# Kernel optimization log

Hardware: AMD Instinct MI355X
Metric: run time of the kernel (lower is better)

## Reference

```python
import jax, jax.numpy as jnp
import numpy as np

S, D, H, DK, DV = 4096, 1024, 16, 64, 64


def setup_inputs() -> dict:
    key = jax.random.key(0)
    ks = jax.random.split(key, 6)
    x = jax.random.normal(ks[0], (S, D), dtype=jnp.float32)
    # per-head projection weights, stacked over heads; scaled for numerical sanity
    Wq = jax.random.normal(ks[1], (H, D, DK), dtype=jnp.float32) / np.sqrt(D)
    Wk = jax.random.normal(ks[2], (H, D, DK), dtype=jnp.float32) / np.sqrt(D)
    Wv = jax.random.normal(ks[3], (H, D, DV), dtype=jnp.float32) / np.sqrt(D)
    Wc = jax.random.normal(ks[4], (H * DV, D), dtype=jnp.float32) / np.sqrt(H * DV)
    bc = jnp.zeros((D,), dtype=jnp.float32)
    return {"x": x, "Wq": Wq, "Wk": Wk, "Wv": Wv, "Wc": Wc, "bc": bc}


def reference(x, Wq, Wk, Wv, Wc, bc):
    # Per-head projections (original loops over heads with separate Linears;
    # stacking over h is the same math, vectorized).
    q = jnp.einsum("sd,hdk->hsk", x, Wq)   # [H,S,DK]
    k = jnp.einsum("sd,hdk->hsk", x, Wk)   # [H,S,DK]
    v = jnp.einsum("sd,hdv->hsv", x, Wv)   # [H,S,DV]
    scores = jnp.einsum("hsk,htk->hst", q, k) / jnp.sqrt(jnp.asarray(DK, x.dtype))
    probs = jax.nn.softmax(scores, axis=-1)  # softmax over last dim, per row
    o = jnp.einsum("hst,htv->hsv", probs, v)  # [H,S,DV]
    cat = jnp.transpose(o, (1, 0, 2)).reshape(S, H * DV)  # concat heads on last dim
    return cat @ Wc + bc  # output projection with bias
```

## Files before the change

kernel.cpp:

```cpp
#include <hip/hip_runtime.h>
#include <hip/hip_bf16.h>

#define S_ 4096
#define D_ 1024
#define H_ 16
#define DK_ 64
#define DV_ 64

typedef short bf16x8 __attribute__((ext_vector_type(8)));
typedef float floatx4 __attribute__((ext_vector_type(4)));
using bf16 = __hip_bfloat16;

#define MFMA16(a, b, c) __builtin_amdgcn_mfma_f32_16x16x32_bf16(a, b, c, 0, 0, 0)

#if __has_builtin(__builtin_amdgcn_exp2f)
#define EXP2(x) __builtin_amdgcn_exp2f(x)
#else
#define EXP2(x) exp2f(x)
#endif

__device__ __forceinline__ void stage16(const void* g, void* l) {
    __builtin_amdgcn_global_load_lds(
        (const __attribute__((address_space(1))) void*)g,
        (__attribute__((address_space(3))) void*)l, 16, 0, 0);
}

__device__ __forceinline__ bf16x8 ldsfrag(const bf16* base, int row, int chunk) {
    return *(const bf16x8*)(base + row * 64 + (((chunk ^ (row & 7))) << 3));
}
__device__ __forceinline__ bf16x8 ldsfrag32(const bf16* base, int row, int chunk) {
    return *(const bf16x8*)(base + row * 32 + (((chunk ^ (row & 3))) << 3));
}

__device__ __forceinline__ unsigned short bfbits(float f) {
    union { bf16 h; unsigned short u; } c; c.h = __float2bfloat16(f); return c.u;
}

__global__ __launch_bounds__(256)
void prep(const float* __restrict__ x, const float* __restrict__ Wq,
          const float* __restrict__ Wk, const float* __restrict__ Wv,
          const float* __restrict__ Wc,
          bf16* __restrict__ xb, bf16* __restrict__ Wt, bf16* __restrict__ Wct)
{
    __shared__ float ls[64][65];
    const int bx = blockIdx.x, t = threadIdx.x;

    if (bx < 2048) {
        int i = bx * 2048 + t * 8;
        float4 a = *(const float4*)(x + i);
        float4 b = *(const float4*)(x + i + 4);
        ushort4 lo, hi;
        lo.x = bfbits(a.x); lo.y = bfbits(a.y); lo.z = bfbits(a.z); lo.w = bfbits(a.w);
        hi.x = bfbits(b.x); hi.y = bfbits(b.y); hi.z = bfbits(b.z); hi.w = bfbits(b.w);
        *(ushort4*)(xb + i) = lo;
        *(ushort4*)(xb + i + 4) = hi;
        return;
    }
    if (bx < 2816) {
        const int idx = bx - 2048;
        const int z = idx >> 4, which = z >> 4, h = z & 15;
        const float* s = (which == 0 ? Wq : which == 1 ? Wk : Wv) + (size_t)h * D_ * 64;
        bf16* d = Wt + ((size_t)which * 1024 + h * 64) * D_;
        const float scale = (which == 0) ? 0.125f * 1.44269504088896340736f : 1.0f;
        const int r0 = (idx & 15) * 64;
        {
            int r = t >> 2, cseg = (t & 3) * 16;
            const float* sp = s + (size_t)(r0 + r) * 64 + cseg;
            #pragma unroll
            for (int i = 0; i < 16; i += 4) {
                float4 v = *(const float4*)(sp + i);
                ls[r][cseg + i + 0] = v.x; ls[r][cseg + i + 1] = v.y;
                ls[r][cseg + i + 2] = v.z; ls[r][cseg + i + 3] = v.w;
            }
        }
        __syncthreads();
        {
            int c = t >> 2, rseg = (t & 3) * 16;
            bf16* dp = d + (size_t)c * D_ + r0 + rseg;
            #pragma unroll
            for (int i = 0; i < 16; i++) dp[i] = __float2bfloat16(ls[rseg + i][c] * scale);
        }
        return;
    }
    {
        const int idx = bx - 2816;
        const int r0 = (idx & 15) * 64, c0 = (idx >> 4) * 64;
        {
            int r = t >> 2, cseg = (t & 3) * 16;
            const float* sp = Wc + (size_t)(r0 + r) * D_ + c0 + cseg;
            #pragma unroll
            for (int i = 0; i < 16; i += 4) {
                float4 v = *(const float4*)(sp + i);
                ls[r][cseg + i + 0] = v.x; ls[r][cseg + i + 1] = v.y;
                ls[r][cseg + i + 2] = v.z; ls[r][cseg + i + 3] = v.w;
            }
        }
        __syncthreads();
        {
            int c = t >> 2, rseg = (t & 3) * 16;
            bf16* dp = Wct + (size_t)(c0 + c) * D_ + r0 + rseg;
            #pragma unroll
            for (int i = 0; i < 16; i++) dp[i] = __float2bfloat16(ls[rseg + i][c]);
        }
    }
}

__global__ __launch_bounds__(256)
void qkv_gemm(const bf16* __restrict__ xb, const bf16* __restrict__ Wt,
              bf16* __restrict__ Qb, bf16* __restrict__ Kb, bf16* __restrict__ Vtb)
{
    const int m0 = blockIdx.x * 128;
    const int n0 = blockIdx.y * 128;
    __shared__ __align__(16) bf16 xa[2][128 * 32];
    __shared__ __align__(16) bf16 wb2[2][128 * 32];

    const int t = threadIdx.x, lane = t & 63, w = t >> 6;
    const int l15 = lane & 15, quad = lane >> 4;

    auto stage_a = [&](int buf, int kk) {
        #pragma unroll
        for (int j = 0; j < 2; j++) {
            int row = j * 64 + (t >> 2);
            int ch  = (t & 3) ^ (row & 3);
            stage16((const char*)xb + ((size_t)(m0 + row) * D_ + kk) * 2 + ch * 16,
                    (char*)&xa[buf][0] + (j * 4 + w) * 1024);
        }
    };
    auto stage_b = [&](int buf, int kk) {
        #pragma unroll
        for (int j = 0; j < 2; j++) {
            int row = j * 64 + (t >> 2);
            int ch  = (t & 3) ^ (row & 3);
            stage16((const char*)Wt + ((size_t)(n0 + row) * D_ + kk) * 2 + ch * 16,
                    (char*)&wb2[buf][0] + (j * 4 + w) * 1024);
        }
    };

    const floatx4 fz = {0.f, 0.f, 0.f, 0.f};
    floatx4 acc[2][8];
    #pragma unroll
    for (int mt = 0; mt < 2; mt++)
        #pragma unroll
        for (int nt = 0; nt < 8; nt++) acc[mt][nt] = fz;

    stage_a(0, 0); stage_b(0, 0);
    for (int kt = 0; kt < 32; kt++) {
        int cur = kt & 1;
        __syncthreads();
        if (kt < 31) { stage_a(cur ^ 1, (kt + 1) * 32); stage_b(cur ^ 1, (kt + 1) * 32); }
        bf16x8 a0 = ldsfrag32(&xa[cur][0], w * 32 + l15,      quad);
        bf16x8 a1 = ldsfrag32(&xa[cur][0], w * 32 + 16 + l15, quad);
        #pragma unroll
        for (int nt = 0; nt < 8; nt++) {
            bf16x8 b = ldsfrag32(&wb2[cur][0], nt * 16 + l15, quad);
            acc[0][nt] = MFMA16(a0, b, acc[0][nt]);
            acc[1][nt] = MFMA16(a1, b, acc[1][nt]);
        }
    }

    const int which = n0 >> 10;
    #pragma unroll
    for (int nt = 0; nt < 8; nt++) {
        int n = n0 + nt * 16 + l15;
        int hh = (n >> 6) & 15, col = n & 63;
        #pragma unroll
        for (int mt = 0; mt < 2; mt++)
            #pragma unroll
            for (int r = 0; r < 4; r++) {
                int s = m0 + w * 32 + mt * 16 + quad * 4 + r;
                bf16 val = __float2bfloat16(acc[mt][nt][r]);
                if (which == 0)      Qb[((size_t)hh * S_ + s) * 64 + col] = val;
                else if (which == 1) Kb[((size_t)hh * S_ + s) * 64 + col] = val;
                else                 Vtb[((size_t)hh * 64 + col) * S_ + s] = val;
            }
    }
}

template<int NKT, bool FULL>
__global__ __launch_bounds__(256, 4)
void attn(const bf16* __restrict__ Qb, const bf16* __restrict__ Kb,
          const bf16* __restrict__ Vtb, bf16* __restrict__ Cat,
          float* __restrict__ Opart, float* __restrict__ lpart)
{
    const int m0 = blockIdx.x * 128;
    const int h  = blockIdx.y;
    const int half = blockIdx.z;
    const int keybase = half * (NKT * 32);

    __shared__ __align__(16) bf16 ka[2][32 * 64];
    __shared__ __align__(16) bf16 vt[2][64 * 32];
    __shared__ __align__(16) bf16 pl[128 * 32];

    const int t = threadIdx.x, lane = t & 63, w = t >> 6;
    const int l15 = lane & 15, quad = lane >> 4;

    auto stage_kv = [&](int buf, int key0) {
        {
            int row = t >> 3;
            int ch  = (t & 7) ^ (row & 7);
            stage16((const char*)(Kb + ((size_t)h * S_ + key0) * 64)
                        + (size_t)row * 128 + ch * 16,
                    (char*)&ka[buf][0] + w * 1024);
        }
        {
            int row = t >> 2;
            int ch  = (t & 3) ^ (row & 3);
            stage16((const char*)(Vtb + (size_t)h * 64 * S_ + key0)
                        + (size_t)row * (S_ * 2) + ch * 16,
                    (char*)&vt[buf][0] + w * 1024);
        }
    };

    bf16x8 qf[2][2];
    #pragma unroll
    for (int nq = 0; nq < 2; nq++)
        #pragma unroll
        for (int ks = 0; ks < 2; ks++)
            qf[nq][ks] = *(const bf16x8*)(Qb +
                ((size_t)h * S_ + m0 + w * 32 + nq * 16 + l15) * 64 + ks * 32 + quad * 8);

    const floatx4 fz = {0.f, 0.f, 0.f, 0.f};
    floatx4 acc[2][4];
    float rs[2] = {0.f, 0.f};
    #pragma unroll
    for (int mt = 0; mt < 2; mt++)
        #pragma unroll
        for (int nt = 0; nt < 4; nt++) acc[mt][nt] = fz;

    const int fq = (l15 >> 2) & 3;
    const int prd0 = (w * 32 + l15) * 64 + ((quad ^ fq) << 4);
    const int prd1 = (w * 32 + 16 + l15) * 64 + ((quad ^ fq) << 4);

    stage_kv(0, keybase);
    __syncthreads();

    for (int kt = 0; kt < NKT; kt++) {
        const int cur = kt & 1;
        if (kt + 1 < NKT) stage_kv(cur ^ 1, keybase + (kt + 1) * 32);

        floatx4 sc[2][2];
        #pragma unroll
        for (int mk = 0; mk < 2; mk++)
            #pragma unroll
            for (int nq = 0; nq < 2; nq++) sc[mk][nq] = fz;
        #pragma unroll
        for (int ks = 0; ks < 2; ks++) {
            bf16x8 af0 = ldsfrag(&ka[cur][0],      l15, ks * 4 + quad);
            bf16x8 af1 = ldsfrag(&ka[cur][0], 16 + l15, ks * 4 + quad);
            #pragma unroll
            for (int nq = 0; nq < 2; nq++) {
                sc[0][nq] = MFMA16(af0, qf[nq][ks], sc[0][nq]);
                sc[1][nq] = MFMA16(af1, qf[nq][ks], sc[1][nq]);
            }
        }

        #pragma unroll
        for (int mk = 0; mk < 2; mk++)
            #pragma unroll
            for (int nq = 0; nq < 2; nq++) {
                float p0 = EXP2(sc[mk][nq][0]);
                float p1 = EXP2(sc[mk][nq][1]);
                float p2 = EXP2(sc[mk][nq][2]);
                float p3 = EXP2(sc[mk][nq][3]);
                rs[nq] += (p0 + p1) + (p2 + p3);
                ushort4 pw;
                pw.x = bfbits(p0); pw.y = bfbits(p1); pw.z = bfbits(p2); pw.w = bfbits(p3);
                int q = w * 32 + nq * 16 + l15;
                int ch = mk * 2 + (quad >> 1);
                *(ushort4*)((char*)pl + q * 64 + ((ch ^ ((q >> 2) & 3)) << 4)
                            + (quad & 1) * 8) = pw;
            }
        asm volatile("s_waitcnt lgkmcnt(0)" ::: "memory");

        bf16x8 a0 = *(const bf16x8*)((const char*)pl + prd0);
        bf16x8 a1 = *(const bf16x8*)((const char*)pl + prd1);
        #pragma unroll
        for (int nt = 0; nt < 4; nt++) {
            bf16x8 b = ldsfrag32(&vt[cur][0], nt * 16 + l15, quad);
            acc[0][nt] = MFMA16(a0, b, acc[0][nt]);
            acc[1][nt] = MFMA16(a1, b, acc[1][nt]);
        }
        __syncthreads();
    }

    __syncthreads();
    float* lsum = (float*)pl;
    #pragma unroll
    for (int nq = 0; nq < 2; nq++) {
        rs[nq] += __shfl_xor(rs[nq], 16);
        rs[nq] += __shfl_xor(rs[nq], 32);
        if (quad == 0) lsum[w * 32 + nq * 16 + l15] = rs[nq];
    }
    asm volatile("s_waitcnt lgkmcnt(0)" ::: "memory");

    if (FULL) {
        #pragma unroll
        for (int mt = 0; mt < 2; mt++)
            #pragma unroll
            for (int r = 0; r < 4; r++) {
                int rl = w * 32 + mt * 16 + quad * 4 + r;
                float inv = 1.0f / lsum[rl];
                #pragma unroll
                for (int nt = 0; nt < 4; nt++)
                    Cat[(size_t)(m0 + rl) * (H_ * DV_) + h * 64 + nt * 16 + l15] =
                        __float2bfloat16(acc[mt][nt][r] * inv);
            }
    } else {
        const size_t plane = (size_t)(half * H_ + h) * S_;
        #pragma unroll
        for (int mt = 0; mt < 2; mt++)
            #pragma unroll
            for (int r = 0; r < 4; r++) {
                int rl = w * 32 + mt * 16 + quad * 4 + r;
                #pragma unroll
                for (int nt = 0; nt < 4; nt++)
                    Opart[(plane + m0 + rl) * 64 + nt * 16 + l15] = acc[mt][nt][r];
            }
        #pragma unroll
        for (int nq = 0; nq < 2; nq++)
            if (quad == 0)
                lpart[plane + m0 + w * 32 + nq * 16 + l15] = rs[nq];
    }
}

__global__ __launch_bounds__(256)
void combine(const float* __restrict__ Opart, const float* __restrict__ lpart,
             bf16* __restrict__ Cat)
{
    const int h = blockIdx.y;
    const int off = blockIdx.x * 1024 + threadIdx.x * 4;
    const int s = off >> 6, dv = off & 63;
    float4 o0 = *(const float4*)(Opart + (size_t)h * S_ * 64 + off);
    float4 o1 = *(const float4*)(Opart + (size_t)(H_ + h) * S_ * 64 + off);
    float inv = 1.0f / (lpart[(size_t)h * S_ + s] + lpart[(size_t)(H_ + h) * S_ + s]);
    ushort4 o;
    o.x = bfbits((o0.x + o1.x) * inv);
    o.y = bfbits((o0.y + o1.y) * inv);
    o.z = bfbits((o0.z + o1.z) * inv);
    o.w = bfbits((o0.w + o1.w) * inv);
    *(ushort4*)(Cat + (size_t)s * (H_ * DV_) + h * 64 + dv) = o;
}

__global__ __launch_bounds__(256)
void out_proj(const bf16* __restrict__ Cat, const bf16* __restrict__ Wct,
              const float* __restrict__ bc, float* __restrict__ out)
{
    const int m0 = blockIdx.x * 128;
    const int n0 = blockIdx.y * 64;
    __shared__ __align__(16) bf16 ca[2][128 * 32];
    __shared__ __align__(16) bf16 wb2[2][64 * 32];

    const int t = threadIdx.x, lane = t & 63, w = t >> 6;
    const int l15 = lane & 15, quad = lane >> 4;

    auto stage_a = [&](int buf, int kk) {
        #pragma unroll
        for (int j = 0; j < 2; j++) {
            int row = j * 64 + (t >> 2);
            int ch  = (t & 3) ^ (row & 3);
            stage16((const char*)Cat + ((size_t)(m0 + row) * D_ + kk) * 2 + ch * 16,
                    (char*)&ca[buf][0] + (j * 4 + w) * 1024);
        }
    };
    auto stage_b = [&](int buf, int kk) {
        int row = t >> 2;
        int ch  = (t & 3) ^ (row & 3);
        stage16((const char*)Wct + ((size_t)(n0 + row) * D_ + kk) * 2 + ch * 16,
                (char*)&wb2[buf][0] + w * 1024);
    };

    const floatx4 fz = {0.f, 0.f, 0.f, 0.f};
    floatx4 acc[2][4];
    #pragma unroll
    for (int mt = 0; mt < 2; mt++)
        #pragma unroll
        for (int nt = 0; nt < 4; nt++) acc[mt][nt] = fz;

    stage_a(0, 0); stage_b(0, 0);
    for (int kt = 0; kt < 32; kt++) {
        int cur = kt & 1;
        __syncthreads();
        if (kt < 31) { stage_a(cur ^ 1, (kt + 1) * 32); stage_b(cur ^ 1, (kt + 1) * 32); }
        bf16x8 a0 = ldsfrag32(&ca[cur][0], w * 32 + l15,      quad);
        bf16x8 a1 = ldsfrag32(&ca[cur][0], w * 32 + 16 + l15, quad);
        #pragma unroll
        for (int nt = 0; nt < 4; nt++) {
            bf16x8 b = ldsfrag32(&wb2[cur][0], nt * 16 + l15, quad);
            acc[0][nt] = MFMA16(a0, b, acc[0][nt]);
            acc[1][nt] = MFMA16(a1, b, acc[1][nt]);
        }
    }

    #pragma unroll
    for (int nt = 0; nt < 4; nt++) {
        int col = n0 + nt * 16 + l15;
        float bias = bc[col];
        #pragma unroll
        for (int mt = 0; mt < 2; mt++)
            #pragma unroll
            for (int r = 0; r < 4; r++) {
                int row = m0 + w * 32 + mt * 16 + quad * 4 + r;
                out[(size_t)row * D_ + col] = acc[mt][nt][r] + bias;
            }
    }
}

extern "C" void kernel_launch(void* const* d_in, const int* in_sizes, int n_in,
                              void* d_out, int out_size, void* d_ws, size_t ws_size,
                              hipStream_t stream)
{
    const float* x  = (const float*)d_in[0];
    const float* Wq = (const float*)d_in[1];
    const float* Wk = (const float*)d_in[2];
    const float* Wv = (const float*)d_in[3];
    const float* Wc = (const float*)d_in[4];
    const float* bc = (const float*)d_in[5];
    float* out = (float*)d_out;

    bf16* xb  = (bf16*)d_ws;
    bf16* Cat = xb;
    bf16* Wt  = xb  + (size_t)S_ * D_;
    bf16* Wct = Wt  + (size_t)3 * H_ * 64 * D_;
    bf16* Qb  = Wct + (size_t)D_ * H_ * DV_;
    bf16* Kb  = Qb  + (size_t)H_ * S_ * 64;
    bf16* Vtb = Kb  + (size_t)H_ * S_ * 64;
    float* Opart = (float*)(Vtb + (size_t)H_ * 64 * S_);
    float* lpart = Opart + (size_t)2 * H_ * S_ * 64;

    const size_t need_split = (size_t)((char*)(lpart + (size_t)2 * H_ * S_) - (char*)d_ws);
    const bool split = ws_size >= need_split;

    prep<<<dim3(3072), 256, 0, stream>>>(x, Wq, Wk, Wv, Wc, xb, Wt, Wct);
    qkv_gemm<<<dim3(S_ / 128, 3072 / 128), 256, 0, stream>>>(xb, Wt, Qb, Kb, Vtb);

    if (split) {
        attn<64, false><<<dim3(S_ / 128, H_, 2), 256, 0, stream>>>(
            Qb, Kb, Vtb, Cat, Opart, lpart);
        combine<<<dim3(S_ * 64 / 1024, H_), 256, 0, stream>>>(Opart, lpart, Cat);
    } else {
        attn<128, true><<<dim3(S_ / 128, H_, 1), 256, 0, stream>>>(
            Qb, Kb, Vtb, Cat, Opart, lpart);
    }

    out_proj<<<dim3(S_ / 128, D_ / 64), 256, 0, stream>>>(Cat, Wct, bc, out);
}
```

Before: 252.5 us.

## Keep softmax probabilities in registers and widen attention key tile

The attention kernel now computes S^T (keys by queries), so each lane's exponentiated scores already sit in the B-operand layout of the P·V MFMA. This removes the LDS round-trip for the probability tile, along with its waitcnt. The key tile grows from 32 to 64 per iteration, which halves the loop trips and barriers but doubles the K/V LDS buffers and the score registers. Output stores become vectorized ushort4/float4 writes, and row sums come straight from shuffles instead of LDS.

```diff
diff --git a/kernel.cpp b/kernel.cpp
--- a/kernel.cpp
+++ b/kernel.cpp
@@ -8,6 +8,7 @@
 #define DV_ 64
 
 typedef short bf16x8 __attribute__((ext_vector_type(8)));
+typedef short bf16x4 __attribute__((ext_vector_type(4)));
 typedef float floatx4 __attribute__((ext_vector_type(4)));
 using bf16 = __hip_bfloat16;
 
@@ -185,29 +186,28 @@
     const int m0 = blockIdx.x * 128;
     const int h  = blockIdx.y;
     const int half = blockIdx.z;
-    const int keybase = half * (NKT * 32);
-
-    __shared__ __align__(16) bf16 ka[2][32 * 64];
-    __shared__ __align__(16) bf16 vt[2][64 * 32];
-    __shared__ __align__(16) bf16 pl[128 * 32];
+    const int keybase = half * (NKT * 64);
+
+    __shared__ __align__(16) bf16 ka[2][64 * 64];
+    __shared__ __align__(16) bf16 vt[2][64 * 64];
 
     const int t = threadIdx.x, lane = t & 63, w = t >> 6;
     const int l15 = lane & 15, quad = lane >> 4;
 
     auto stage_kv = [&](int buf, int key0) {
-        {
-            int row = t >> 3;
-            int ch  = (t & 7) ^ (row & 7);
-            stage16((const char*)(Kb + ((size_t)h * S_ + key0) * 64)
-                        + (size_t)row * 128 + ch * 16,
-                    (char*)&ka[buf][0] + w * 1024);
-        }
-        {
-            int row = t >> 2;
-            int ch  = (t & 3) ^ (row & 3);
-            stage16((const char*)(Vtb + (size_t)h * 64 * S_ + key0)
-                        + (size_t)row * (S_ * 2) + ch * 16,
-                    (char*)&vt[buf][0] + w * 1024);
+        const char* kg = (const char*)(Kb + ((size_t)h * S_ + key0) * 64);
+        #pragma unroll
+        for (int j = 0; j < 2; j++) {
+            int c = (j * 4 + w) * 64 + lane;
+            int row = c >> 3, ch = (c & 7) ^ (row & 7);
+            stage16(kg + row * 128 + ch * 16, (char*)&ka[buf][0] + (j * 4 + w) * 1024);
+        }
+        const char* vg = (const char*)(Vtb + (size_t)h * 64 * S_ + key0);
+        #pragma unroll
+        for (int j = 0; j < 2; j++) {
+            int c = (j * 4 + w) * 64 + lane;
+            int row = c >> 3, ch = (c & 7) ^ (row & 7);
+            stage16(vg + (size_t)row * (S_ * 2) + ch * 16, (char*)&vt[buf][0] + (j * 4 + w) * 1024);
         }
     };
 
@@ -223,39 +223,38 @@
     floatx4 acc[2][4];
     float rs[2] = {0.f, 0.f};
     #pragma unroll
-    for (int mt = 0; mt < 2; mt++)
-        #pragma unroll
-        for (int nt = 0; nt < 4; nt++) acc[mt][nt] = fz;
-
-    const int fq = (l15 >> 2) & 3;
-    const int prd0 = (w * 32 + l15) * 64 + ((quad ^ fq) << 4);
-    const int prd1 = (w * 32 + 16 + l15) * 64 + ((quad ^ fq) << 4);
+    for (int nq = 0; nq < 2; nq++)
+        #pragma unroll
+        for (int nt = 0; nt < 4; nt++) acc[nq][nt] = fz;
 
     stage_kv(0, keybase);
     __syncthreads();
 
     for (int kt = 0; kt < NKT; kt++) {
         const int cur = kt & 1;
-        if (kt + 1 < NKT) stage_kv(cur ^ 1, keybase + (kt + 1) * 32);
-
-        floatx4 sc[2][2];
-        #pragma unroll
-        for (int mk = 0; mk < 2; mk++)
+        if (kt + 1 < NKT) stage_kv(cur ^ 1, keybase + (kt + 1) * 64);
+
+        floatx4 sc[4][2];
+        #pragma unroll
+        for (int mk = 0; mk < 4; mk++)
             #pragma unroll
             for (int nq = 0; nq < 2; nq++) sc[mk][nq] = fz;
         #pragma unroll
         for (int ks = 0; ks < 2; ks++) {
-            bf16x8 af0 = ldsfrag(&ka[cur][0],      l15, ks * 4 + quad);
-            bf16x8 af1 = ldsfrag(&ka[cur][0], 16 + l15, ks * 4 + quad);
-            #pragma unroll
-            for (int nq = 0; nq < 2; nq++) {
-                sc[0][nq] = MFMA16(af0, qf[nq][ks], sc[0][nq]);
-                sc[1][nq] = MFMA16(af1, qf[nq][ks], sc[1][nq]);
-            }
-        }
-
-        #pragma unroll
-        for (int mk = 0; mk < 2; mk++)
+            bf16x8 af[4];
+            #pragma unroll
+            for (int mk = 0; mk < 4; mk++)
+                af[mk] = ldsfrag(&ka[cur][0], mk * 16 + l15, ks * 4 + quad);
+            #pragma unroll
+            for (int mk = 0; mk < 4; mk++)
+                #pragma unroll
+                for (int nq = 0; nq < 2; nq++)
+                    sc[mk][nq] = MFMA16(af[mk], qf[nq][ks], sc[mk][nq]);
+        }
+
+        bf16x4 pf[4][2];
+        #pragma unroll
+        for (int mk = 0; mk < 4; mk++)
             #pragma unroll
             for (int nq = 0; nq < 2; nq++) {
                 float p0 = EXP2(sc[mk][nq][0]);
@@ -263,63 +262,70 @@
                 float p2 = EXP2(sc[mk][nq][2]);
                 float p3 = EXP2(sc[mk][nq][3]);
                 rs[nq] += (p0 + p1) + (p2 + p3);
-                ushort4 pw;
-                pw.x = bfbits(p0); pw.y = bfbits(p1); pw.z = bfbits(p2); pw.w = bfbits(p3);
-                int q = w * 32 + nq * 16 + l15;
-                int ch = mk * 2 + (quad >> 1);
-                *(ushort4*)((char*)pl + q * 64 + ((ch ^ ((q >> 2) & 3)) << 4)
-                            + (quad & 1) * 8) = pw;
-            }
-        asm volatile("s_waitcnt lgkmcnt(0)" ::: "memory");
-
-        bf16x8 a0 = *(const bf16x8*)((const char*)pl + prd0);
-        bf16x8 a1 = *(const bf16x8*)((const char*)pl + prd1);
-        #pragma unroll
-        for (int nt = 0; nt < 4; nt++) {
-            bf16x8 b = ldsfrag32(&vt[cur][0], nt * 16 + l15, quad);
-            acc[0][nt] = MFMA16(a0, b, acc[0][nt]);
-            acc[1][nt] = MFMA16(a1, b, acc[1][nt]);
+                union { bf16x4 v; unsigned short e[4]; } u;
+                u.e[0] = bfbits(p0); u.e[1] = bfbits(p1);
+                u.e[2] = bfbits(p2); u.e[3] = bfbits(p3);
+                pf[mk][nq] = u.v;
+            }
+
+        #pragma unroll
+        for (int p = 0; p < 2; p++) {
+            union { bf16x8 v8; bf16x4 v4[2]; } b8[2];
+            #pragma unroll
+            for (int nq = 0; nq < 2; nq++) {
+                b8[nq].v4[0] = pf[2 * p + 0][nq];
+                b8[nq].v4[1] = pf[2 * p + 1][nq];
+            }
+            #pragma unroll
+            for (int nt = 0; nt < 4; nt++) {
+                const char* vb = (const char*)&vt[cur][0]
+                               + (nt * 16 + l15) * 128 + (quad & 1) * 8;
+                const int r7 = l15 & 7;
+                union { bf16x8 v8; bf16x4 v4[2]; } a8;
+                a8.v4[0] = *(const bf16x4*)(vb + (((4 * p +     (quad >> 1)) ^ r7) << 4));
+                a8.v4[1] = *(const bf16x4*)(vb + (((4 * p + 2 + (quad >> 1)) ^ r7) << 4));
+                #pragma unroll
+                for (int nq = 0; nq < 2; nq++)
+                    acc[nq][nt] = MFMA16(a8.v8, b8[nq].v8, acc[nq][nt]);
+            }
         }
         __syncthreads();
     }
 
-    __syncthreads();
-    float* lsum = (float*)pl;
     #pragma unroll
     for (int nq = 0; nq < 2; nq++) {
         rs[nq] += __shfl_xor(rs[nq], 16);
         rs[nq] += __shfl_xor(rs[nq], 32);
-        if (quad == 0) lsum[w * 32 + nq * 16 + l15] = rs[nq];
-    }
-    asm volatile("s_waitcnt lgkmcnt(0)" ::: "memory");
+    }
 
     if (FULL) {
         #pragma unroll
-        for (int mt = 0; mt < 2; mt++)
-            #pragma unroll
-            for (int r = 0; r < 4; r++) {
-                int rl = w * 32 + mt * 16 + quad * 4 + r;
-                float inv = 1.0f / lsum[rl];
-                #pragma unroll
-                for (int nt = 0; nt < 4; nt++)
-                    Cat[(size_t)(m0 + rl) * (H_ * DV_) + h * 64 + nt * 16 + l15] =
-                        __float2bfloat16(acc[mt][nt][r] * inv);
-            }
+        for (int nq = 0; nq < 2; nq++) {
+            float inv = 1.0f / rs[nq];
+            int q = m0 + w * 32 + nq * 16 + l15;
+            #pragma unroll
+            for (int nt = 0; nt < 4; nt++) {
+                ushort4 o;
+                o.x = bfbits(acc[nq][nt][0] * inv);
+                o.y = bfbits(acc[nq][nt][1] * inv);
+                o.z = bfbits(acc[nq][nt][2] * inv);
+                o.w = bfbits(acc[nq][nt][3] * inv);
+                *(ushort4*)(Cat + (size_t)q * (H_ * DV_) + h * 64 + nt * 16 + quad * 4) = o;
+            }
+        }
     } else {
         const size_t plane = (size_t)(half * H_ + h) * S_;
         #pragma unroll
-        for (int mt = 0; mt < 2; mt++)
-            #pragma unroll
-            for (int r = 0; r < 4; r++) {
-                int rl = w * 32 + mt * 16 + quad * 4 + r;
-                #pragma unroll
-                for (int nt = 0; nt < 4; nt++)
-                    Opart[(plane + m0 + rl) * 64 + nt * 16 + l15] = acc[mt][nt][r];
-            }
-        #pragma unroll
-        for (int nq = 0; nq < 2; nq++)
-            if (quad == 0)
-                lpart[plane + m0 + w * 32 + nq * 16 + l15] = rs[nq];
+        for (int nq = 0; nq < 2; nq++) {
+            int q = m0 + w * 32 + nq * 16 + l15;
+            #pragma unroll
+            for (int nt = 0; nt < 4; nt++) {
+                float4 o = { acc[nq][nt][0], acc[nq][nt][1],
+                             acc[nq][nt][2], acc[nq][nt][3] };
+                *(float4*)(Opart + (plane + q) * 64 + nt * 16 + quad * 4) = o;
+            }
+            if (quad == 0) lpart[plane + q] = rs[nq];
+        }
     }
 }
 
@@ -434,11 +440,11 @@
     qkv_gemm<<<dim3(S_ / 128, 3072 / 128), 256, 0, stream>>>(xb, Wt, Qb, Kb, Vtb);
 
     if (split) {
-        attn<64, false><<<dim3(S_ / 128, H_, 2), 256, 0, stream>>>(
+        attn<32, false><<<dim3(S_ / 128, H_, 2), 256, 0, stream>>>(
             Qb, Kb, Vtb, Cat, Opart, lpart);
         combine<<<dim3(S_ * 64 / 1024, H_), 256, 0, stream>>>(Opart, lpart, Cat);
     } else {
-        attn<128, true><<<dim3(S_ / 128, H_, 1), 256, 0, stream>>>(
+        attn<64, true><<<dim3(S_ / 128, H_, 1), 256, 0, stream>>>(
             Qb, Kb, Vtb, Cat, Opart, lpart);
     }
 
```

After: 241.3 us. -4.4%, faster.
